# Kernel optimization log

Measured on AMD Instinct MI355X. Metric: run time of the kernel, lower is better.

Reference implementation:

```python
import jax, jax.numpy as jnp
import numpy as np

BN_EPS = 1e-5

def setup_inputs() -> dict:
    key = jax.random.key(0)
    ks = jax.random.split(key, 16)
    B, H, W, C = 4, 64, 64, 256
    N = H * W                      # 4096 tokens
    heads, sr = 8, 2
    Nk = (H // sr) * (W // sr)     # 1024 reduced KV tokens
    s = 0.02
    return {
        "x": jax.random.normal(ks[0], (B, N, C), jnp.float32),
        "H": H,
        "W": W,
        "relative_pos": jax.random.normal(ks[1], (heads, N, Nk), jnp.float32),
        # linear weights, torch layout [out, in]; q/k/v have no bias (qkv_bias=False)
        "q_w": jax.random.normal(ks[2], (C, C), jnp.float32) * s,
        "k_w": jax.random.normal(ks[3], (C, C), jnp.float32) * s,
        "v_w": jax.random.normal(ks[4], (C, C), jnp.float32) * s,
        "proj_w": jax.random.normal(ks[5], (C, C), jnp.float32) * s,
        "proj_b": jnp.zeros((C,), jnp.float32),
        # depthwise conv (groups=C): OIHW with I=1
        "sr_w": jax.random.normal(ks[6], (C, 1, sr, sr), jnp.float32) * s,
        "sr_b": jnp.zeros((C,), jnp.float32),
        # BatchNorm2d (eval mode) params/buffers
        "bn_gamma": jnp.ones((C,), jnp.float32),
        "bn_beta": jnp.zeros((C,), jnp.float32),
        "bn_mean": jax.random.normal(ks[7], (C,), jnp.float32) * 0.1,
        "bn_var": jax.random.uniform(ks[8], (C,), jnp.float32, 0.5, 1.5),
    }


def reference(x, H, W, relative_pos, q_w, k_w, v_w, proj_w, proj_b,
              sr_w, sr_b, bn_gamma, bn_beta, bn_mean, bn_var):
    B, N, C = x.shape
    heads = relative_pos.shape[0]
    qk_dim = q_w.shape[0]
    dh = qk_dim // heads
    dv = C // heads
    scale = dh ** -0.5
    sr = sr_w.shape[-1]

    # q: [B, heads, N, dh]
    q = (x @ q_w.T).reshape(B, N, heads, dh).transpose(0, 2, 1, 3)

    # spatial reduction: depthwise conv stride sr + BatchNorm (eval)
    x_img = x.transpose(0, 2, 1).reshape(B, C, H, W)
    xk = jax.lax.conv_general_dilated(
        x_img, sr_w, window_strides=(sr, sr), padding='VALID',
        feature_group_count=C,
        dimension_numbers=('NCHW', 'OIHW', 'NCHW')) + sr_b[None, :, None, None]
    inv_std = bn_gamma / jnp.sqrt(bn_var + BN_EPS)
    xk = (xk - bn_mean[None, :, None, None]) * inv_std[None, :, None, None] \
         + bn_beta[None, :, None, None]
    Nk = xk.shape[2] * xk.shape[3]
    xk = xk.reshape(B, C, Nk).transpose(0, 2, 1)   # [B, Nk, C]

    k = (xk @ k_w.T).reshape(B, Nk, heads, dh).transpose(0, 2, 1, 3)
    v = (xk @ v_w.T).reshape(B, Nk, heads, dv).transpose(0, 2, 1, 3)

    # scores + additive relative position bias, softmax, weighted sum
    attn = jnp.einsum('bhnd,bhmd->bhnm', q, k) * scale + relative_pos[None]
    attn = jax.nn.softmax(attn, axis=-1)
    out = jnp.einsum('bhnm,bhmd->bhnd', attn, v)
    out = out.transpose(0, 2, 1, 3).reshape(B, N, C)
    return out @ proj_w.T + proj_b
```

## Files before the change

kernel.cpp:

```cpp
#include <hip/hip_runtime.h>
#include <cstdint>
#include <cstddef>

#define DEV static __device__ __forceinline__

typedef __bf16 bf16x8 __attribute__((ext_vector_type(8)));
typedef __bf16 bf16x4 __attribute__((ext_vector_type(4)));
typedef float  f32x4  __attribute__((ext_vector_type(4)));
typedef unsigned short us4 __attribute__((ext_vector_type(4)));
typedef unsigned int   u32x4 __attribute__((ext_vector_type(4)));

DEV unsigned short f2bf(float f) {
  unsigned u = __float_as_uint(f);
  u += 0x7FFFu + ((u >> 16) & 1u);
  return (unsigned short)(u >> 16);
}

constexpr int   Bn = 4, Nn = 4096, Cn = 256, HEADSn = 8, DHn = 32, NKn = 1024;
constexpr float SCALEc = 0.17677669529663689f;
constexpr float L2E    = 1.4426950408889634f;

__global__ void k_f32_to_bf16(const float* __restrict__ src,
                              unsigned short* __restrict__ dst, int n4, float scale) {
  int i = blockIdx.x * blockDim.x + threadIdx.x;
  if (i < n4) {
    f32x4 v = *(const f32x4*)(src + 4 * (size_t)i);
    us4 o;
    o[0] = f2bf(v[0] * scale); o[1] = f2bf(v[1] * scale);
    o[2] = f2bf(v[2] * scale); o[3] = f2bf(v[3] * scale);
    *(us4*)(dst + 4 * (size_t)i) = o;
  }
}

__global__ void k_conv_bn(const float* __restrict__ x,
                          const float* __restrict__ srw, const float* __restrict__ srb,
                          const float* __restrict__ bng, const float* __restrict__ bnb,
                          const float* __restrict__ bnm, const float* __restrict__ bnv,
                          unsigned short* __restrict__ xk) {
  const int m = blockIdx.x;
  const int b = blockIdx.y;
  const int c = threadIdx.x;
  const int i = m >> 5, j = m & 31;
  const int n00 = (2 * i) * 64 + 2 * j;
  const size_t base = ((size_t)b * Nn) * Cn + c;
  float w0 = srw[c * 4 + 0], w1 = srw[c * 4 + 1], w2 = srw[c * 4 + 2], w3 = srw[c * 4 + 3];
  float acc = x[base + (size_t)n00 * Cn] * w0
            + x[base + (size_t)(n00 + 1) * Cn] * w1
            + x[base + (size_t)(n00 + 64) * Cn] * w2
            + x[base + (size_t)(n00 + 65) * Cn] * w3
            + srb[c];
  float inv_std = bng[c] * rsqrtf(bnv[c] + 1e-5f);
  acc = (acc - bnm[c]) * inv_std + bnb[c];
  xk[((size_t)b * NKn + m) * Cn + c] = f2bf(acc);
}

template <int MODE>
__global__ __launch_bounds__(256) void k_gemm(const unsigned short* __restrict__ A,
                                              const unsigned short* __restrict__ W,
                                              void* __restrict__ outp,
                                              const float* __restrict__ bias, int rs) {
  __shared__ __align__(16) unsigned short sA[64 * 256];
  __shared__ __align__(16) unsigned short sW[64 * 256];
  const int tid = threadIdx.x;
  const int lane = tid & 63, w = tid >> 6;
  const int g = lane >> 4, c = lane & 15;
  const int m0 = blockIdx.x * 64, o0 = blockIdx.y * 64;

#pragma unroll
  for (int r = 0; r < 8; ++r) {
    const int row = r * 8 + (tid >> 5);
    const int u = tid & 31;
    const int usw = u ^ (row & 7);
    bf16x8 va = *(const bf16x8*)(A + (size_t)(m0 + row) * Cn + u * 8);
    *(bf16x8*)(sA + row * Cn + usw * 8) = va;
    bf16x8 vw = *(const bf16x8*)(W + (size_t)(o0 + row) * Cn + u * 8);
    *(bf16x8*)(sW + row * Cn + usw * 8) = vw;
  }
  __syncthreads();

  f32x4 acc[4] = {};
  const int rowa = w * 16 + c;
#pragma unroll
  for (int ks = 0; ks < 8; ++ks) {
    bf16x8 af = *(const bf16x8*)(sA + rowa * Cn + ((ks * 4 + g) ^ (c & 7)) * 8);
#pragma unroll
    for (int t = 0; t < 4; ++t) {
      const int roww = 16 * t + c;
      bf16x8 wf = *(const bf16x8*)(sW + roww * Cn + ((ks * 4 + g) ^ (c & 7)) * 8);
      acc[t] = __builtin_amdgcn_mfma_f32_16x16x32_bf16(af, wf, acc[t], 0, 0, 0);
    }
  }

  const int mb = m0 + w * 16;
  if (MODE == 0) {
    unsigned short* ob = (unsigned short*)outp;
#pragma unroll
    for (int t = 0; t < 4; ++t)
#pragma unroll
      for (int r = 0; r < 4; ++r)
        ob[(size_t)(mb + 4 * g + r) * Cn + o0 + 16 * t + c] = f2bf(acc[t][r]);
  } else if (MODE == 1) {
    unsigned short* vt = (unsigned short*)outp;
    const int m4 = mb + 4 * g;
    const int b = m4 >> 10;
    const int kvblk = (m4 & 1023) >> 5;
    const int jh = (m4 >> 4) & 1;
#pragma unroll
    for (int t = 0; t < 4; ++t) {
      const int o = o0 + 16 * t + c;
      const int h = o >> 5, dv = o & 31;
      us4 pk;
      pk[0] = f2bf(acc[t][0]); pk[1] = f2bf(acc[t][1]);
      pk[2] = f2bf(acc[t][2]); pk[3] = f2bf(acc[t][3]);
      *(us4*)(vt + ((size_t)(((b * 8 + h) * 32 + kvblk) * 32 + dv)) * 32 + g * 8 + jh * 4) = pk;
    }
  } else if (MODE == 2) {
    float* of = (float*)outp;
#pragma unroll
    for (int t = 0; t < 4; ++t) {
      const int o = o0 + 16 * t + c;
      const float bv = bias[o];
#pragma unroll
      for (int r = 0; r < 4; ++r)
        of[(size_t)(mb + 4 * g + r) * Cn + o] = acc[t][r] + bv;
    }
  } else {
    unsigned short* ot = (unsigned short*)outp;
#pragma unroll
    for (int t = 0; t < 4; ++t) {
      const int o = o0 + 16 * t + c;
      const int h = o >> 5, dh = o & 31;
#pragma unroll
      for (int r = 0; r < 4; ++r) {
        const int m = mb + 4 * g + r;
        const int b = m >> rs, rl = m & ((1 << rs) - 1);
        ot[((size_t)(((b * 8 + h) << rs) + rl)) * 32 + dh] = f2bf(acc[t][r]);
      }
    }
  }
}

__global__ __launch_bounds__(512, 2) void k_attn(const unsigned short* __restrict__ qt,
                                                 const unsigned short* __restrict__ kt,
                                                 const unsigned short* __restrict__ vt,
                                                 const float* __restrict__ rel,
                                                 unsigned short* __restrict__ ob) {
  __shared__ __align__(16) char s_rel[2][16384];
  const int tid = threadIdx.x;
  const int lane = tid & 63, w = tid >> 6;
  const int bb = w & 3, qh = w >> 2;
  const int g = lane >> 4, c = lane & 15;
  const int h = blockIdx.x >> 5;
  const int q0 = (blockIdx.x & 31) * 128;

  const int srow = tid >> 2, su2 = (tid & 3) * 2;
  const float* sgp = rel + ((size_t)h * Nn + q0 + srow) * NKn + su2 * 4;
  int swo[2];
#pragma unroll
  for (int j = 0; j < 2; ++j) swo[j] = srow * 128 + (((su2 + j) ^ (srow & 7)) << 4);
  char* sb = &s_rel[0][0];

  bf16x8 qf[4];
#pragma unroll
  for (int t = 0; t < 4; ++t)
    qf[t] = *(const bf16x8*)(qt + ((size_t)((bb * 8 + h) << 12) + q0 + qh * 64 + 16 * t + c) * 32 + 8 * g);

  bf16x8 ones;
#pragma unroll
  for (int r = 0; r < 8; ++r) ones[r] = (__bf16)1.0f;

  f32x4 acc[4][2] = {};
  f32x4 accl[4] = {};

  const unsigned short* kbase = kt + ((size_t)((bb * 8 + h) << 10)) * 32 + 8 * g;
  const unsigned short* vbase = vt + ((size_t)(bb * 8 + h) * 1024) * 32;

  auto sub = [&](const char* rb, int t, bf16x8 k0, bf16x8 k1, bf16x8 v0, bf16x8 v1) {
    f32x4 zero = {};
    f32x4 s0 = __builtin_amdgcn_mfma_f32_16x16x32_bf16(k0, qf[t], zero, 0, 0, 0);
    f32x4 s1 = __builtin_amdgcn_mfma_f32_16x16x32_bf16(k1, qf[t], zero, 0, 0, 0);
    const int rrow = (qh * 64 + 16 * t + c) * 128;
    f32x4 r0 = *(const f32x4*)(rb + rrow + ((g ^ (c & 7)) << 4));
    f32x4 r1 = *(const f32x4*)(rb + rrow + (((4 + g) ^ (c & 7)) << 4));
    s0 += r0 * L2E;
    s1 += r1 * L2E;
    float p0[4], p1[4];
#pragma unroll
    for (int r = 0; r < 4; ++r) {
      p0[r] = __builtin_amdgcn_exp2f(s0[r]);
      p1[r] = __builtin_amdgcn_exp2f(s1[r]);
    }
    u32x4 pw;
    pw[0] = __builtin_amdgcn_perm(__float_as_uint(p0[1]), __float_as_uint(p0[0]), 0x07060302u);
    pw[1] = __builtin_amdgcn_perm(__float_as_uint(p0[3]), __float_as_uint(p0[2]), 0x07060302u);
    pw[2] = __builtin_amdgcn_perm(__float_as_uint(p1[1]), __float_as_uint(p1[0]), 0x07060302u);
    pw[3] = __builtin_amdgcn_perm(__float_as_uint(p1[3]), __float_as_uint(p1[2]), 0x07060302u);
    bf16x8 pf = __builtin_bit_cast(bf16x8, pw);
    accl[t] = __builtin_amdgcn_mfma_f32_16x16x32_bf16(ones, pf, accl[t], 0, 0, 0);
    acc[t][0] = __builtin_amdgcn_mfma_f32_16x16x32_bf16(v0, pf, acc[t][0], 0, 0, 0);
    acc[t][1] = __builtin_amdgcn_mfma_f32_16x16x32_bf16(v1, pf, acc[t][1], 0, 0, 0);
  };

  auto tile = [&](int e, int rbuf,
                  bf16x8& k0c, bf16x8& k1c, bf16x8& v0c, bf16x8& v1c,
                  bf16x8& k0n, bf16x8& k1n, bf16x8& v0n, bf16x8& v1n,
                  f32x4& S0, f32x4& S1) {
    char* wb = sb + (rbuf ^ 1) * 16384;
    *(f32x4*)(wb + swo[0]) = S0;
    *(f32x4*)(wb + swo[1]) = S1;
    const int kvn = ((e + 1) & 31) * 32;
    k0n = *(const bf16x8*)(kbase + (size_t)(kvn + c) * 32);
    k1n = *(const bf16x8*)(kbase + (size_t)(kvn + 16 + c) * 32);
    v0n = *(const bf16x8*)(vbase + (size_t)(kvn + c) * 32 + g * 8);
    v1n = *(const bf16x8*)(vbase + (size_t)(kvn + 16 + c) * 32 + g * 8);
    __builtin_amdgcn_sched_barrier(0);
    const char* rb = sb + rbuf * 16384;
#pragma unroll
    for (int t = 0; t < 4; ++t) sub(rb, t, k0c, k1c, v0c, v1c);
    const int rn = ((e + 3) & 31) * 32;
    S0 = *(const f32x4*)(sgp + rn);
    S1 = *(const f32x4*)(sgp + rn + 4);
  };

  {
    f32x4 t0 = *(const f32x4*)(sgp);
    f32x4 t1 = *(const f32x4*)(sgp + 4);
    *(f32x4*)(sb + swo[0]) = t0;
    *(f32x4*)(sb + swo[1]) = t1;
  }
  f32x4 SA0 = *(const f32x4*)(sgp + 32);
  f32x4 SA1 = *(const f32x4*)(sgp + 36);
  f32x4 SB0 = *(const f32x4*)(sgp + 64);
  f32x4 SB1 = *(const f32x4*)(sgp + 68);
  bf16x8 kP0 = *(const bf16x8*)(kbase + (size_t)(c) * 32);
  bf16x8 kP1 = *(const bf16x8*)(kbase + (size_t)(16 + c) * 32);
  bf16x8 vP0 = *(const bf16x8*)(vbase + (size_t)(c) * 32 + g * 8);
  bf16x8 vP1 = *(const bf16x8*)(vbase + (size_t)(16 + c) * 32 + g * 8);
  bf16x8 kQ0, kQ1, vQ0, vQ1;
  __syncthreads();

  for (int ee = 0; ee < 32; ee += 2) {
    tile(ee, 0, kP0, kP1, vP0, vP1, kQ0, kQ1, vQ0, vQ1, SA0, SA1);
    __syncthreads();
    tile(ee + 1, 1, kQ0, kQ1, vQ0, vQ1, kP0, kP1, vP0, vP1, SB0, SB1);
    __syncthreads();
  }

#pragma unroll
  for (int t = 0; t < 4; ++t) {
    const float inv = 1.0f / accl[t][0];
#pragma unroll
    for (int hh = 0; hh < 2; ++hh) {
      us4 pk;
      pk[0] = f2bf(acc[t][hh][0] * inv);
      pk[1] = f2bf(acc[t][hh][1] * inv);
      pk[2] = f2bf(acc[t][hh][2] * inv);
      pk[3] = f2bf(acc[t][hh][3] * inv);
      *(us4*)(ob + ((size_t)bb * Nn + q0 + qh * 64 + 16 * t + c) * Cn + h * DHn + hh * 16 + 4 * g) = pk;
    }
  }
}

extern "C" void kernel_launch(void* const* d_in, const int* in_sizes, int n_in,
                              void* d_out, int out_size, void* d_ws, size_t ws_size,
                              hipStream_t stream) {
  const float* x   = (const float*)d_in[0];
  const float* rel = (const float*)d_in[3];
  const float* qw  = (const float*)d_in[4];
  const float* kw  = (const float*)d_in[5];
  const float* vw  = (const float*)d_in[6];
  const float* pw  = (const float*)d_in[7];
  const float* pb  = (const float*)d_in[8];
  const float* srw = (const float*)d_in[9];
  const float* srb = (const float*)d_in[10];
  const float* bng = (const float*)d_in[11];
  const float* bnb = (const float*)d_in[12];
  const float* bnm = (const float*)d_in[13];
  const float* bnv = (const float*)d_in[14];

  char* ws = (char*)d_ws;
  unsigned short* x_bf  = (unsigned short*)(ws + 0);
  unsigned short* q_t   = (unsigned short*)(ws + 8388608);
  unsigned short* xk_bf = (unsigned short*)(ws + 16777216);
  unsigned short* k_t   = (unsigned short*)(ws + 18874368);
  unsigned short* v_2   = (unsigned short*)(ws + 20971520);
  unsigned short* a_bf  = (unsigned short*)(ws + 23068672);
  unsigned short* w_q   = (unsigned short*)(ws + 31457280);
  unsigned short* w_k   = (unsigned short*)(ws + 31457280 + 131072);
  unsigned short* w_v   = (unsigned short*)(ws + 31457280 + 262144);
  unsigned short* w_p   = (unsigned short*)(ws + 31457280 + 393216);

  k_f32_to_bf16<<<4096, 256, 0, stream>>>(x, x_bf, 1048576, 1.0f);
  k_f32_to_bf16<<<64, 256, 0, stream>>>(qw, w_q, 16384, SCALEc * L2E);
  k_f32_to_bf16<<<64, 256, 0, stream>>>(kw, w_k, 16384, 1.0f);
  k_f32_to_bf16<<<64, 256, 0, stream>>>(vw, w_v, 16384, 1.0f);
  k_f32_to_bf16<<<64, 256, 0, stream>>>(pw, w_p, 16384, 1.0f);

  k_conv_bn<<<dim3(1024, 4), 256, 0, stream>>>(x, srw, srb, bng, bnb, bnm, bnv, xk_bf);

  k_gemm<3><<<dim3(256, 4), 256, 0, stream>>>(x_bf, w_q, (void*)q_t, nullptr, 12);
  k_gemm<3><<<dim3(64, 4), 256, 0, stream>>>(xk_bf, w_k, (void*)k_t, nullptr, 10);
  k_gemm<1><<<dim3(64, 4), 256, 0, stream>>>(xk_bf, w_v, (void*)v_2, nullptr, 0);

  k_attn<<<dim3(256), 512, 0, stream>>>(q_t, k_t, v_2, rel, a_bf);

  k_gemm<2><<<dim3(256, 4), 256, 0, stream>>>(a_bf, w_p, d_out, pb, 0);
}
```

Before: 80.87 us.

## Fuse x bf16 conversion into Q GEMM, merge K/V GEMMs and weight casts

Measured after the change: 72.49 us (median of 2 runs). 10.4% less time.

```diff
diff --git a/kernel.cpp b/kernel.cpp
--- a/kernel.cpp
+++ b/kernel.cpp
@@ -8,6 +8,7 @@
 typedef __bf16 bf16x4 __attribute__((ext_vector_type(4)));
 typedef float  f32x4  __attribute__((ext_vector_type(4)));
 typedef unsigned short us4 __attribute__((ext_vector_type(4)));
+typedef unsigned short us8 __attribute__((ext_vector_type(8)));
 typedef unsigned int   u32x4 __attribute__((ext_vector_type(4)));
 
 DEV unsigned short f2bf(float f) {
@@ -20,16 +21,20 @@
 constexpr float SCALEc = 0.17677669529663689f;
 constexpr float L2E    = 1.4426950408889634f;
 
-__global__ void k_f32_to_bf16(const float* __restrict__ src,
-                              unsigned short* __restrict__ dst, int n4, float scale) {
-  int i = blockIdx.x * blockDim.x + threadIdx.x;
-  if (i < n4) {
-    f32x4 v = *(const f32x4*)(src + 4 * (size_t)i);
-    us4 o;
-    o[0] = f2bf(v[0] * scale); o[1] = f2bf(v[1] * scale);
-    o[2] = f2bf(v[2] * scale); o[3] = f2bf(v[3] * scale);
-    *(us4*)(dst + 4 * (size_t)i) = o;
-  }
+__global__ void k_cvt_w(const float* __restrict__ qw, const float* __restrict__ kw,
+                        const float* __restrict__ vw, const float* __restrict__ pw,
+                        unsigned short* __restrict__ wq, unsigned short* __restrict__ wk,
+                        unsigned short* __restrict__ wv, unsigned short* __restrict__ wp) {
+  const int which = blockIdx.x >> 6;
+  const int i = (blockIdx.x & 63) * 256 + threadIdx.x;
+  const float* src = which == 0 ? qw : which == 1 ? kw : which == 2 ? vw : pw;
+  unsigned short* dst = which == 0 ? wq : which == 1 ? wk : which == 2 ? wv : wp;
+  const float scale = which == 0 ? SCALEc * L2E : 1.0f;
+  f32x4 v = *(const f32x4*)(src + 4 * (size_t)i);
+  us4 o;
+  o[0] = f2bf(v[0] * scale); o[1] = f2bf(v[1] * scale);
+  o[2] = f2bf(v[2] * scale); o[3] = f2bf(v[3] * scale);
+  *(us4*)(dst + 4 * (size_t)i) = o;
 }
 
 __global__ void k_conv_bn(const float* __restrict__ x,
@@ -54,8 +59,8 @@
   xk[((size_t)b * NKn + m) * Cn + c] = f2bf(acc);
 }
 
-template <int MODE>
-__global__ __launch_bounds__(256) void k_gemm(const unsigned short* __restrict__ A,
+template <int MODE, bool AF32>
+__global__ __launch_bounds__(256) void k_gemm(const void* __restrict__ Ap,
                                               const unsigned short* __restrict__ W,
                                               void* __restrict__ outp,
                                               const float* __restrict__ bias, int rs) {
@@ -71,8 +76,19 @@
     const int row = r * 8 + (tid >> 5);
     const int u = tid & 31;
     const int usw = u ^ (row & 7);
-    bf16x8 va = *(const bf16x8*)(A + (size_t)(m0 + row) * Cn + u * 8);
-    *(bf16x8*)(sA + row * Cn + usw * 8) = va;
+    if (AF32) {
+      const float* af = (const float*)Ap;
+      f32x4 lo = *(const f32x4*)(af + (size_t)(m0 + row) * Cn + u * 8);
+      f32x4 hi = *(const f32x4*)(af + (size_t)(m0 + row) * Cn + u * 8 + 4);
+      us8 pk;
+      pk[0] = f2bf(lo[0]); pk[1] = f2bf(lo[1]); pk[2] = f2bf(lo[2]); pk[3] = f2bf(lo[3]);
+      pk[4] = f2bf(hi[0]); pk[5] = f2bf(hi[1]); pk[6] = f2bf(hi[2]); pk[7] = f2bf(hi[3]);
+      *(us8*)(sA + row * Cn + usw * 8) = pk;
+    } else {
+      const unsigned short* ab = (const unsigned short*)Ap;
+      bf16x8 va = *(const bf16x8*)(ab + (size_t)(m0 + row) * Cn + u * 8);
+      *(bf16x8*)(sA + row * Cn + usw * 8) = va;
+    }
     bf16x8 vw = *(const bf16x8*)(W + (size_t)(o0 + row) * Cn + u * 8);
     *(bf16x8*)(sW + row * Cn + usw * 8) = vw;
   }
@@ -92,29 +108,7 @@
   }
 
   const int mb = m0 + w * 16;
-  if (MODE == 0) {
-    unsigned short* ob = (unsigned short*)outp;
-#pragma unroll
-    for (int t = 0; t < 4; ++t)
-#pragma unroll
-      for (int r = 0; r < 4; ++r)
-        ob[(size_t)(mb + 4 * g + r) * Cn + o0 + 16 * t + c] = f2bf(acc[t][r]);
-  } else if (MODE == 1) {
-    unsigned short* vt = (unsigned short*)outp;
-    const int m4 = mb + 4 * g;
-    const int b = m4 >> 10;
-    const int kvblk = (m4 & 1023) >> 5;
-    const int jh = (m4 >> 4) & 1;
-#pragma unroll
-    for (int t = 0; t < 4; ++t) {
-      const int o = o0 + 16 * t + c;
-      const int h = o >> 5, dv = o & 31;
-      us4 pk;
-      pk[0] = f2bf(acc[t][0]); pk[1] = f2bf(acc[t][1]);
-      pk[2] = f2bf(acc[t][2]); pk[3] = f2bf(acc[t][3]);
-      *(us4*)(vt + ((size_t)(((b * 8 + h) * 32 + kvblk) * 32 + dv)) * 32 + g * 8 + jh * 4) = pk;
-    }
-  } else if (MODE == 2) {
+  if (MODE == 2) {
     float* of = (float*)outp;
 #pragma unroll
     for (int t = 0; t < 4; ++t) {
@@ -136,6 +130,77 @@
         const int b = m >> rs, rl = m & ((1 << rs) - 1);
         ot[((size_t)(((b * 8 + h) << rs) + rl)) * 32 + dh] = f2bf(acc[t][r]);
       }
+    }
+  }
+}
+
+__global__ __launch_bounds__(256) void k_gemm_kv(const unsigned short* __restrict__ xk,
+                                                 const unsigned short* __restrict__ Wk,
+                                                 const unsigned short* __restrict__ Wv,
+                                                 unsigned short* __restrict__ kt,
+                                                 unsigned short* __restrict__ vt) {
+  __shared__ __align__(16) unsigned short sA[64 * 256];
+  __shared__ __align__(16) unsigned short sWk[64 * 256];
+  __shared__ __align__(16) unsigned short sWv[64 * 256];
+  const int tid = threadIdx.x;
+  const int lane = tid & 63, w = tid >> 6;
+  const int g = lane >> 4, c = lane & 15;
+  const int m0 = blockIdx.x * 64, o0 = blockIdx.y * 64;
+
+#pragma unroll
+  for (int r = 0; r < 8; ++r) {
+    const int row = r * 8 + (tid >> 5);
+    const int u = tid & 31;
+    const int usw = u ^ (row & 7);
+    bf16x8 va = *(const bf16x8*)(xk + (size_t)(m0 + row) * Cn + u * 8);
+    *(bf16x8*)(sA + row * Cn + usw * 8) = va;
+    bf16x8 vk = *(const bf16x8*)(Wk + (size_t)(o0 + row) * Cn + u * 8);
+    *(bf16x8*)(sWk + row * Cn + usw * 8) = vk;
+    bf16x8 vv = *(const bf16x8*)(Wv + (size_t)(o0 + row) * Cn + u * 8);
+    *(bf16x8*)(sWv + row * Cn + usw * 8) = vv;
+  }
+  __syncthreads();
+
+  f32x4 ak[4] = {}, av[4] = {};
+  const int rowa = w * 16 + c;
+#pragma unroll
+  for (int ks = 0; ks < 8; ++ks) {
+    bf16x8 af = *(const bf16x8*)(sA + rowa * Cn + ((ks * 4 + g) ^ (c & 7)) * 8);
+#pragma unroll
+    for (int t = 0; t < 4; ++t) {
+      const int roww = 16 * t + c;
+      bf16x8 wkf = *(const bf16x8*)(sWk + roww * Cn + ((ks * 4 + g) ^ (c & 7)) * 8);
+      ak[t] = __builtin_amdgcn_mfma_f32_16x16x32_bf16(af, wkf, ak[t], 0, 0, 0);
+      bf16x8 wvf = *(const bf16x8*)(sWv + roww * Cn + ((ks * 4 + g) ^ (c & 7)) * 8);
+      av[t] = __builtin_amdgcn_mfma_f32_16x16x32_bf16(af, wvf, av[t], 0, 0, 0);
+    }
+  }
+
+  const int mb = m0 + w * 16;
+#pragma unroll
+  for (int t = 0; t < 4; ++t) {
+    const int o = o0 + 16 * t + c;
+    const int h = o >> 5, dh = o & 31;
+#pragma unroll
+    for (int r = 0; r < 4; ++r) {
+      const int m = mb + 4 * g + r;
+      const int b = m >> 10, rl = m & 1023;
+      kt[((size_t)(((b * 8 + h) << 10) + rl)) * 32 + dh] = f2bf(ak[t][r]);
+    }
+  }
+  {
+    const int m4 = mb + 4 * g;
+    const int b = m4 >> 10;
+    const int kvblk = (m4 & 1023) >> 5;
+    const int jh = (m4 >> 4) & 1;
+#pragma unroll
+    for (int t = 0; t < 4; ++t) {
+      const int o = o0 + 16 * t + c;
+      const int h = o >> 5, dv = o & 31;
+      us4 pk;
+      pk[0] = f2bf(av[t][0]); pk[1] = f2bf(av[t][1]);
+      pk[2] = f2bf(av[t][2]); pk[3] = f2bf(av[t][3]);
+      *(us4*)(vt + ((size_t)(((b * 8 + h) * 32 + kvblk) * 32 + dv)) * 32 + g * 8 + jh * 4) = pk;
     }
   }
 }
@@ -279,30 +344,25 @@
   const float* bnv = (const float*)d_in[14];
 
   char* ws = (char*)d_ws;
-  unsigned short* x_bf  = (unsigned short*)(ws + 0);
-  unsigned short* q_t   = (unsigned short*)(ws + 8388608);
-  unsigned short* xk_bf = (unsigned short*)(ws + 16777216);
-  unsigned short* k_t   = (unsigned short*)(ws + 18874368);
-  unsigned short* v_2   = (unsigned short*)(ws + 20971520);
-  unsigned short* a_bf  = (unsigned short*)(ws + 23068672);
-  unsigned short* w_q   = (unsigned short*)(ws + 31457280);
-  unsigned short* w_k   = (unsigned short*)(ws + 31457280 + 131072);
-  unsigned short* w_v   = (unsigned short*)(ws + 31457280 + 262144);
-  unsigned short* w_p   = (unsigned short*)(ws + 31457280 + 393216);
-
-  k_f32_to_bf16<<<4096, 256, 0, stream>>>(x, x_bf, 1048576, 1.0f);
-  k_f32_to_bf16<<<64, 256, 0, stream>>>(qw, w_q, 16384, SCALEc * L2E);
-  k_f32_to_bf16<<<64, 256, 0, stream>>>(kw, w_k, 16384, 1.0f);
-  k_f32_to_bf16<<<64, 256, 0, stream>>>(vw, w_v, 16384, 1.0f);
-  k_f32_to_bf16<<<64, 256, 0, stream>>>(pw, w_p, 16384, 1.0f);
+  unsigned short* q_t   = (unsigned short*)(ws + 0);
+  unsigned short* xk_bf = (unsigned short*)(ws + 8388608);
+  unsigned short* k_t   = (unsigned short*)(ws + 10485760);
+  unsigned short* v_2   = (unsigned short*)(ws + 12582912);
+  unsigned short* a_bf  = (unsigned short*)(ws + 14680064);
+  unsigned short* w_q   = (unsigned short*)(ws + 23068672);
+  unsigned short* w_k   = (unsigned short*)(ws + 23068672 + 131072);
+  unsigned short* w_v   = (unsigned short*)(ws + 23068672 + 262144);
+  unsigned short* w_p   = (unsigned short*)(ws + 23068672 + 393216);
+
+  k_cvt_w<<<256, 256, 0, stream>>>(qw, kw, vw, pw, w_q, w_k, w_v, w_p);
 
   k_conv_bn<<<dim3(1024, 4), 256, 0, stream>>>(x, srw, srb, bng, bnb, bnm, bnv, xk_bf);
 
-  k_gemm<3><<<dim3(256, 4), 256, 0, stream>>>(x_bf, w_q, (void*)q_t, nullptr, 12);
-  k_gemm<3><<<dim3(64, 4), 256, 0, stream>>>(xk_bf, w_k, (void*)k_t, nullptr, 10);
-  k_gemm<1><<<dim3(64, 4), 256, 0, stream>>>(xk_bf, w_v, (void*)v_2, nullptr, 0);
+  k_gemm<3, true><<<dim3(256, 4), 256, 0, stream>>>((const void*)x, w_q, (void*)q_t, nullptr, 12);
+
+  k_gemm_kv<<<dim3(64, 4), 256, 0, stream>>>(xk_bf, w_k, w_v, k_t, v_2);
 
   k_attn<<<dim3(256), 512, 0, stream>>>(q_t, k_t, v_2, rel, a_bf);
 
-  k_gemm<2><<<dim3(256, 4), 256, 0, stream>>>(a_bf, w_p, d_out, pb, 0);
-}
+  k_gemm<2, false><<<dim3(256, 4), 256, 0, stream>>>((const void*)a_bf, w_p, d_out, pb, 0);
+}
```
